# Kernel tuning notes

Hardware: AMD Instinct MI355X
Metric: run time of the kernel (lower is better)

Reference implementation:

```python
import jax, jax.numpy as jnp
import numpy as np

B, L, N_IN, NUM_CLASS = 2, 256, 128, 1
INIT_STD = 0.01


def setup_inputs() -> dict:
    key = jax.random.key(0)
    kx, ky, kz, kw = jax.random.split(key, 4)
    x = jax.random.normal(kx, (B, L, N_IN), dtype=jnp.float32)
    y = jax.random.normal(ky, (B, L, N_IN), dtype=jnp.float32)
    z = jax.random.normal(kz, (B, L, N_IN), dtype=jnp.float32)
    # weight: [n_in + bias_x, n_in, n_in + bias_y, num_class], init ~ N(0, init_std)
    weight = jax.random.normal(kw, (N_IN + 1, N_IN, N_IN + 1, NUM_CLASS), dtype=jnp.float32) * INIT_STD
    return {"x": x, "y": y, "z": z, "weight": weight}


def reference(x, y, z, weight):
    # bias_x / bias_y: append a ones column to x and y
    xb = jnp.concatenate([x, jnp.ones_like(x[..., :1])], axis=-1)  # [B, L, n_in+1]
    yb = jnp.concatenate([y, jnp.ones_like(y[..., :1])], axis=-1)  # [B, L, n_in+1]
    # 4-way triaffine contraction -> [B, Lx, Ly, Lz, r]
    s = jnp.einsum('bxi,bzk,ikjr,byj->bxyzr', xb, z, weight, yb, optimize=True)
    # num_class == 1: squeeze last dim (original returns before applying scale)
    return s[..., 0]
```

## Files before the change

### kernel.cpp

```cpp
#include <hip/hip_runtime.h>


typedef __bf16 bf16x8 __attribute__((ext_vector_type(8)));
typedef short short4_t __attribute__((ext_vector_type(4)));
typedef float f32x4 __attribute__((ext_vector_type(4)));
typedef unsigned short ushort4_t __attribute__((ext_vector_type(4)));

#define LL 256
#define NI 128
#define NFLATP 17408
#define KJ_STRIDE 136
#define XB_STRIDE 132
#define P_STRIDE 132

__device__ __forceinline__ unsigned short f2bf(float f) {
    unsigned u = __builtin_bit_cast(unsigned, f);
    u += 0x7FFFu + ((u >> 16) & 1u);
    return (unsigned short)(u >> 16);
}
__device__ __forceinline__ float bf2f(unsigned short h) {
    return __builtin_bit_cast(float, (unsigned)h << 16);
}

__global__ __launch_bounds__(512, 4) void stage1_kernel(const float* __restrict__ W,
                                                        const float* __restrict__ x,
                                                        const float* __restrict__ y,
                                                        const float* __restrict__ z,
                                                        unsigned short* __restrict__ yzbf,
                                                        unsigned short* __restrict__ A2g) {
    const int blk = blockIdx.x, tid = threadIdx.x;

    if (blk >= 272) {
        int t = (blk - 272) * 512 + tid;
        int base = t * 4;
        int which = base >> 16;
        int local = base & 65535;
        const float* s = which ? z : y;
        float4 v = *(const float4*)(s + local);
        ushort4_t o;
        o[0] = f2bf(v.x); o[1] = f2bf(v.y); o[2] = f2bf(v.z); o[3] = f2bf(v.w);
        *(ushort4_t*)(yzbf + base) = o;
        return;
    }

    __shared__ unsigned short T[128 * KJ_STRIDE];
    __shared__ unsigned short XB[128 * XB_STRIDE];

    const int wv = tid >> 6, lane = tid & 63;
    const int l15 = lane & 15, h = lane >> 4;

    {
        const int nl = tid & 127, ig = tid >> 7;
        const int np = (blk >> 1) * 128 + nl;
        const int k  = np / KJ_STRIDE;
        const int j  = np - k * KJ_STRIDE;
        const bool jok = (j <= 128);
        const float* Wkj = W + (size_t)k * 129 + j;
        float wreg[33];
#pragma unroll
        for (int r = 0; r < 33; ++r) {
            int i = ig + r * 4;
            wreg[r] = (i <= 128 && jok) ? Wkj[(size_t)i * 16512] : 0.f;
        }
#pragma unroll
        for (int r = 0; r < 33; ++r) {
            int i = ig + r * 4;
            if (i <= 128) T[nl * KJ_STRIDE + i] = f2bf(wreg[r]);
        }
    }
    __syncthreads();

    const int bxg = blk & 1;
    const int nb  = blk >> 1;
    const int nloc  = wv * 16;
    const int nglob = nb * 128 + nloc;

    bf16x8 af[4];
#pragma unroll
    for (int is = 0; is < 4; ++is)
        af[is] = *(const bf16x8*)&T[(nloc + l15) * KJ_STRIDE + is * 32 + 8 * h];
    f32x4 binit;
#pragma unroll
    for (int r = 0; r < 4; ++r)
        binit[r] = bf2f(T[(nloc + 4 * h + r) * KJ_STRIDE + 128]);

#pragma unroll 1
    for (int sp = 0; sp < 2; ++sp) {
        if (sp) __syncthreads();
        const int bx0 = bxg * 256 + sp * 128;

        {
            const float* xsrc = x + (size_t)bx0 * NI;
#pragma unroll
            for (int c = 0; c < 8; ++c) {
                int idx = c * 512 + tid;
                float4 v = *(const float4*)(xsrc + (size_t)idx * 4);
                int row = idx >> 5, col = (idx & 31) * 4;
                ushort4_t o;
                o[0] = f2bf(v.x); o[1] = f2bf(v.y); o[2] = f2bf(v.z); o[3] = f2bf(v.w);
                *(ushort4_t*)&XB[row * XB_STRIDE + col] = o;
            }
        }
        __syncthreads();

        f32x4 acc[8];
#pragma unroll
        for (int ct = 0; ct < 8; ++ct) acc[ct] = binit;
#pragma unroll
        for (int is = 0; is < 4; ++is)
#pragma unroll
            for (int ct = 0; ct < 8; ++ct) {
                bf16x8 xf = *(const bf16x8*)&XB[(ct * 16 + l15) * XB_STRIDE + is * 32 + 8 * h];
                acc[ct] = __builtin_amdgcn_mfma_f32_16x16x32_bf16(af[is], xf, acc[ct], 0, 0, 0);
            }
#pragma unroll
        for (int ct = 0; ct < 8; ++ct) {
            ushort4_t o;
#pragma unroll
            for (int r = 0; r < 4; ++r) o[r] = f2bf(acc[ct][r]);
            *(ushort4_t*)(A2g + (size_t)(bx0 + ct * 16 + l15) * NFLATP + nglob + 4 * h) = o;
        }
    }
}

__global__ __launch_bounds__(512, 4) void stage2_kernel(const unsigned short* __restrict__ ybf,
                                                        const unsigned short* __restrict__ zbf,
                                                        const unsigned short* __restrict__ A2g,
                                                        float* __restrict__ out) {
    const int bx  = blockIdx.x;
    const int b   = bx >> 8;
    const int tid = threadIdx.x;
    const int wv = tid >> 6, lane = tid & 63;
    const int l15 = lane & 15, h = lane >> 4;

    __shared__ __align__(16) unsigned short SH[LL * P_STRIDE];

    {
        const float4* src = (const float4*)(A2g + (size_t)bx * NFLATP);
        float4* dst = (float4*)SH;
        for (int t = tid; t < NFLATP / 8; t += 512) dst[t] = src[t];
    }
    __syncthreads();

    const unsigned short* yb = ybf + b * LL * NI;
    const unsigned short* zb = zbf + b * LL * NI;
    const int y0 = wv * 32;

    f32x4 accP[8][2];
#pragma unroll
    for (int kt = 0; kt < 8; ++kt)
#pragma unroll
        for (int r = 0; r < 4; ++r) {
            float bias = bf2f(SH[(kt * 16 + 4 * h + r) * KJ_STRIDE + 128]);
            accP[kt][0][r] = bias; accP[kt][1][r] = bias;
        }
#pragma unroll
    for (int js = 0; js < 4; ++js) {
        bf16x8 yf[2];
#pragma unroll
        for (int yt = 0; yt < 2; ++yt)
            yf[yt] = *(const bf16x8*)(yb + (y0 + yt * 16 + l15) * NI + js * 32 + 8 * h);
#pragma unroll
        for (int kt = 0; kt < 8; ++kt) {
            bf16x8 af2 = *(const bf16x8*)&SH[(kt * 16 + l15) * KJ_STRIDE + js * 32 + 8 * h];
            accP[kt][0] = __builtin_amdgcn_mfma_f32_16x16x32_bf16(af2, yf[0], accP[kt][0], 0, 0, 0);
            accP[kt][1] = __builtin_amdgcn_mfma_f32_16x16x32_bf16(af2, yf[1], accP[kt][1], 0, 0, 0);
        }
    }
    __syncthreads();

#pragma unroll
    for (int kt = 0; kt < 8; ++kt)
#pragma unroll
        for (int yt = 0; yt < 2; ++yt) {
            unsigned lo = (unsigned)f2bf(accP[kt][yt][0]) | ((unsigned)f2bf(accP[kt][yt][1]) << 16);
            unsigned hi = (unsigned)f2bf(accP[kt][yt][2]) | ((unsigned)f2bf(accP[kt][yt][3]) << 16);
            uint2 v; v.x = lo; v.y = hi;
            *(uint2*)&SH[(y0 + yt * 16 + l15) * P_STRIDE + kt * 16 + 4 * h] = v;
        }

    const int zg = wv & 3, yh = wv >> 2;
    const int z0 = zg * 64;
    short4_t zf[4][8];
#pragma unroll
    for (int zt = 0; zt < 4; ++zt)
#pragma unroll
        for (int kt = 0; kt < 8; ++kt)
            zf[zt][kt] = *(const short4_t*)(zb + (z0 + zt * 16 + l15) * NI + kt * 16 + 4 * h);

    __syncthreads();

    float* outb = out + (size_t)bx * (LL * LL);
#pragma unroll 1
    for (int yti = 0; yti < 8; ++yti) {
        const int yy = yh * 128 + yti * 16 + l15;
        f32x4 acc2[4];
#pragma unroll
        for (int zt = 0; zt < 4; ++zt) { acc2[zt][0] = 0.f; acc2[zt][1] = 0.f; acc2[zt][2] = 0.f; acc2[zt][3] = 0.f; }
#pragma unroll
        for (int kt = 0; kt < 8; ++kt) {
            short4_t pB = *(const short4_t*)&SH[yy * P_STRIDE + kt * 16 + 4 * h];
#pragma unroll
            for (int zt = 0; zt < 4; ++zt)
                acc2[zt] = __builtin_amdgcn_mfma_f32_16x16x16bf16_1k(zf[zt][kt], pB, acc2[zt], 0, 0, 0);
        }
#pragma unroll
        for (int zt = 0; zt < 4; ++zt)
            *(f32x4*)(outb + (size_t)yy * LL + z0 + zt * 16 + 4 * h) = acc2[zt];
    }
}

extern "C" void kernel_launch(void* const* d_in, const int* in_sizes, int n_in,
                              void* d_out, int out_size, void* d_ws, size_t ws_size,
                              hipStream_t stream) {
    const float* x = (const float*)d_in[0];
    const float* y = (const float*)d_in[1];
    const float* z = (const float*)d_in[2];
    const float* W = (const float*)d_in[3];
    float* out = (float*)d_out;

    unsigned short* yzbf = (unsigned short*)d_ws;
    unsigned short* A2g  = yzbf + 131072;

    stage1_kernel<<<336, 512, 0, stream>>>(W, x, y, z, yzbf, A2g);
    stage2_kernel<<<512, 512, 0, stream>>>(yzbf, yzbf + 65536, A2g, out);
}
```

Measured before the change: 67.46 us.

## Process two x-rows per stage2 block, reusing z fragments and prefetching second A2 slice

```diff
diff --git a/kernel.cpp b/kernel.cpp
--- a/kernel.cpp
+++ b/kernel.cpp
@@ -123,28 +123,35 @@
     }
 }
 
-__global__ __launch_bounds__(512, 4) void stage2_kernel(const unsigned short* __restrict__ ybf,
+__global__ __launch_bounds__(512, 2) void stage2_kernel(const unsigned short* __restrict__ ybf,
                                                         const unsigned short* __restrict__ zbf,
                                                         const unsigned short* __restrict__ A2g,
                                                         float* __restrict__ out) {
-    const int bx  = blockIdx.x;
-    const int b   = bx >> 8;
+    const int blk = blockIdx.x;
+    const int bxa = blk * 2, bxb = bxa + 1;
+    const int b   = bxa >> 8;
     const int tid = threadIdx.x;
     const int wv = tid >> 6, lane = tid & 63;
     const int l15 = lane & 15, h = lane >> 4;
 
-    __shared__ __align__(16) unsigned short SH[LL * P_STRIDE];
-
-    {
-        const float4* src = (const float4*)(A2g + (size_t)bx * NFLATP);
-        float4* dst = (float4*)SH;
-        for (int t = tid; t < NFLATP / 8; t += 512) dst[t] = src[t];
+    __shared__ __align__(16) unsigned short SH[LL * P_STRIDE + NFLATP];
+    unsigned short* R1 = SH + LL * P_STRIDE;
+
+    {
+        const float4* sa = (const float4*)(A2g + (size_t)bxa * NFLATP);
+        const float4* sb = (const float4*)(A2g + (size_t)bxb * NFLATP);
+        float4* d0 = (float4*)SH;
+        float4* d1 = (float4*)R1;
+        for (int t = tid; t < NFLATP / 8; t += 512) d0[t] = sa[t];
+        for (int t = tid; t < NFLATP / 8; t += 512) d1[t] = sb[t];
     }
     __syncthreads();
 
     const unsigned short* yb = ybf + b * LL * NI;
     const unsigned short* zb = zbf + b * LL * NI;
     const int y0 = wv * 32;
+    const int zg = wv & 3, yh = wv >> 2;
+    const int z0 = zg * 64;
 
     f32x4 accP[8][2];
 #pragma unroll
@@ -178,35 +185,87 @@
             uint2 v; v.x = lo; v.y = hi;
             *(uint2*)&SH[(y0 + yt * 16 + l15) * P_STRIDE + kt * 16 + 4 * h] = v;
         }
-
-    const int zg = wv & 3, yh = wv >> 2;
-    const int z0 = zg * 64;
     short4_t zf[4][8];
 #pragma unroll
     for (int zt = 0; zt < 4; ++zt)
 #pragma unroll
         for (int kt = 0; kt < 8; ++kt)
             zf[zt][kt] = *(const short4_t*)(zb + (z0 + zt * 16 + l15) * NI + kt * 16 + 4 * h);
-
-    __syncthreads();
-
-    float* outb = out + (size_t)bx * (LL * LL);
+    __syncthreads();
+
+    {
+        float* outb = out + (size_t)bxa * (LL * LL);
 #pragma unroll 1
-    for (int yti = 0; yti < 8; ++yti) {
-        const int yy = yh * 128 + yti * 16 + l15;
-        f32x4 acc2[4];
-#pragma unroll
-        for (int zt = 0; zt < 4; ++zt) { acc2[zt][0] = 0.f; acc2[zt][1] = 0.f; acc2[zt][2] = 0.f; acc2[zt][3] = 0.f; }
+        for (int yti = 0; yti < 8; ++yti) {
+            const int yy = yh * 128 + yti * 16 + l15;
+            f32x4 acc2[4];
+#pragma unroll
+            for (int zt = 0; zt < 4; ++zt) { acc2[zt][0] = 0.f; acc2[zt][1] = 0.f; acc2[zt][2] = 0.f; acc2[zt][3] = 0.f; }
+#pragma unroll
+            for (int kt = 0; kt < 8; ++kt) {
+                short4_t pB = *(const short4_t*)&SH[yy * P_STRIDE + kt * 16 + 4 * h];
+#pragma unroll
+                for (int zt = 0; zt < 4; ++zt)
+                    acc2[zt] = __builtin_amdgcn_mfma_f32_16x16x16bf16_1k(zf[zt][kt], pB, acc2[zt], 0, 0, 0);
+            }
+#pragma unroll
+            for (int zt = 0; zt < 4; ++zt)
+                *(f32x4*)(outb + (size_t)yy * LL + z0 + zt * 16 + 4 * h) = acc2[zt];
+        }
+    }
+
+#pragma unroll
+    for (int kt = 0; kt < 8; ++kt)
+#pragma unroll
+        for (int r = 0; r < 4; ++r) {
+            float bias = bf2f(R1[(kt * 16 + 4 * h + r) * KJ_STRIDE + 128]);
+            accP[kt][0][r] = bias; accP[kt][1][r] = bias;
+        }
+#pragma unroll
+    for (int js = 0; js < 4; ++js) {
+        bf16x8 yf[2];
+#pragma unroll
+        for (int yt = 0; yt < 2; ++yt)
+            yf[yt] = *(const bf16x8*)(yb + (y0 + yt * 16 + l15) * NI + js * 32 + 8 * h);
 #pragma unroll
         for (int kt = 0; kt < 8; ++kt) {
-            short4_t pB = *(const short4_t*)&SH[yy * P_STRIDE + kt * 16 + 4 * h];
+            bf16x8 af2 = *(const bf16x8*)&R1[(kt * 16 + l15) * KJ_STRIDE + js * 32 + 8 * h];
+            accP[kt][0] = __builtin_amdgcn_mfma_f32_16x16x32_bf16(af2, yf[0], accP[kt][0], 0, 0, 0);
+            accP[kt][1] = __builtin_amdgcn_mfma_f32_16x16x32_bf16(af2, yf[1], accP[kt][1], 0, 0, 0);
+        }
+    }
+    __syncthreads();
+
+#pragma unroll
+    for (int kt = 0; kt < 8; ++kt)
+#pragma unroll
+        for (int yt = 0; yt < 2; ++yt) {
+            unsigned lo = (unsigned)f2bf(accP[kt][yt][0]) | ((unsigned)f2bf(accP[kt][yt][1]) << 16);
+            unsigned hi = (unsigned)f2bf(accP[kt][yt][2]) | ((unsigned)f2bf(accP[kt][yt][3]) << 16);
+            uint2 v; v.x = lo; v.y = hi;
+            *(uint2*)&SH[(y0 + yt * 16 + l15) * P_STRIDE + kt * 16 + 4 * h] = v;
+        }
+    __syncthreads();
+
+    {
+        float* outb = out + (size_t)bxb * (LL * LL);
+#pragma unroll 1
+        for (int yti = 0; yti < 8; ++yti) {
+            const int yy = yh * 128 + yti * 16 + l15;
+            f32x4 acc2[4];
+#pragma unroll
+            for (int zt = 0; zt < 4; ++zt) { acc2[zt][0] = 0.f; acc2[zt][1] = 0.f; acc2[zt][2] = 0.f; acc2[zt][3] = 0.f; }
+#pragma unroll
+            for (int kt = 0; kt < 8; ++kt) {
+                short4_t pB = *(const short4_t*)&SH[yy * P_STRIDE + kt * 16 + 4 * h];
+#pragma unroll
+                for (int zt = 0; zt < 4; ++zt)
+                    acc2[zt] = __builtin_amdgcn_mfma_f32_16x16x16bf16_1k(zf[zt][kt], pB, acc2[zt], 0, 0, 0);
+            }
 #pragma unroll
             for (int zt = 0; zt < 4; ++zt)
-                acc2[zt] = __builtin_amdgcn_mfma_f32_16x16x16bf16_1k(zf[zt][kt], pB, acc2[zt], 0, 0, 0);
-        }
-#pragma unroll
-        for (int zt = 0; zt < 4; ++zt)
-            *(f32x4*)(outb + (size_t)yy * LL + z0 + zt * 16 + 4 * h) = acc2[zt];
+                *(f32x4*)(outb + (size_t)yy * LL + z0 + zt * 16 + 4 * h) = acc2[zt];
+        }
     }
 }
 
@@ -223,5 +282,5 @@
     unsigned short* A2g  = yzbf + 131072;
 
     stage1_kernel<<<336, 512, 0, stream>>>(W, x, y, z, yzbf, A2g);
-    stage2_kernel<<<512, 512, 0, stream>>>(yzbf, yzbf + 65536, A2g, out);
-}
+    stage2_kernel<<<256, 512, 0, stream>>>(yzbf, yzbf + 65536, A2g, out);
+}
```

Result: faster. 64.01 us, median of 2 (-5.1%).
